# Kernel tuning notes

Hardware: AMD Instinct MI355X
Metric: run time of the kernel (lower is better)

The kernel has to match this reference:

```python
import jax, jax.numpy as jnp
import numpy as np

B, T = 128, 64          # batch, episode length
OB, AC, L, H = 32, 8, 128, 256  # ob_dim, ac_dim, latent_dim, mlp hidden
N_SUB = 4               # fixed Dopri5 substeps per interval (replaces adaptive PID controller)


def setup_inputs() -> dict:
    key = jax.random.key(0)
    ks = jax.random.split(key, 12)
    g = lambda k, shape, fan: jax.random.normal(k, shape, jnp.float32) / np.sqrt(fan)
    return {
        "ob": jax.random.normal(ks[0], (B, OB), jnp.float32),
        "acs": jax.random.normal(ks[1], (B, T, AC), jnp.float32),
        # strictly increasing timestamps (cumsum of uniform increments)
        "times": jnp.cumsum(jax.random.uniform(ks[2], (B, T), jnp.float32, 0.02, 0.1), axis=1),
        # ob encoder MLP (OB -> H -> L), relu hidden, identity out
        "We0": g(ks[3], (H, OB), OB), "be0": jnp.zeros((H,), jnp.float32),
        "We1": g(ks[4], (L, H), H), "be1": jnp.zeros((L,), jnp.float32),
        # latent dynamics MLP (L -> H -> H -> L)
        "Wd0": g(ks[5], (H, L), L), "bd0": jnp.zeros((H,), jnp.float32),
        "Wd1": g(ks[6], (H, H), H), "bd1": jnp.zeros((H,), jnp.float32),
        "Wd2": g(ks[7], (L, H), H), "bd2": jnp.zeros((L,), jnp.float32),
        # ob decoder MLP (L -> H -> OB)
        "Wo0": g(ks[8], (H, L), L), "bo0": jnp.zeros((H,), jnp.float32),
        "Wo1": g(ks[9], (OB, H), H), "bo1": jnp.zeros((OB,), jnp.float32),
        # GRU cell (input=AC, hidden=L), equinox layout: gates [r, z, n]
        "Wih": g(ks[10], (3 * L, AC), AC), "Whh": g(ks[11], (3 * L, L), L),
        "bih": jnp.zeros((3 * L,), jnp.float32), "bn": jnp.zeros((L,), jnp.float32),
    }


def reference(ob, acs, times, We0, be0, We1, be1, Wd0, bd0, Wd1, bd1, Wd2, bd2,
              Wo0, bo0, Wo1, bo1, Wih, Whh, bih, bn):
    def f(y):  # dynamics MLP on batched latent (B, L) -> (B, L)
        h1 = jax.nn.relu(y @ Wd0.T + bd0)
        h2 = jax.nn.relu(h1 @ Wd1.T + bd1)
        return h2 @ Wd2.T + bd2

    def gru(x, h):  # equinox GRUCell math, batched
        ir, iz, inn = jnp.split(x @ Wih.T + bih, 3, axis=-1)
        hr, hz, hn = jnp.split(h @ Whh.T, 3, axis=-1)
        r = jax.nn.sigmoid(ir + hr)
        z = jax.nn.sigmoid(iz + hz)
        n = jnp.tanh(inn + r * (hn + bn))
        return (1.0 - z) * n + z * h

    def dopri5_step(y, h):  # one Dopri5 (RK45) step, h: (B, 1) per-sample step size
        k1 = f(y)
        k2 = f(y + h * (0.2 * k1))
        k3 = f(y + h * (3/40 * k1 + 9/40 * k2))
        k4 = f(y + h * (44/45 * k1 - 56/15 * k2 + 32/9 * k3))
        k5 = f(y + h * (19372/6561 * k1 - 25360/2187 * k2 + 64448/6561 * k3 - 212/729 * k4))
        k6 = f(y + h * (9017/3168 * k1 - 355/33 * k2 + 46732/5247 * k3 + 49/176 * k4 - 5103/18656 * k5))
        return y + h * (35/384 * k1 + 500/1113 * k3 + 125/192 * k4 - 2187/6784 * k5 + 11/84 * k6)

    def integrate(y, dt):  # integrate latent ODE from 0 to dt with N_SUB fixed Dopri5 steps
        h = (dt / N_SUB)[:, None]
        return jax.lax.fori_loop(0, N_SUB, lambda i, yy: dopri5_step(yy, h), y)

    # encode first observation, consume first action
    latent0 = jax.nn.relu(ob @ We0.T + be0) @ We1.T + be1  # (B, L)
    latent0 = gru(acs[:, 0], latent0)

    dts = jnp.diff(times, axis=1)  # (B, T-1)

    def step(latent, xs):
        ac, dt = xs
        latent = integrate(latent, dt)
        latent = gru(ac, latent)
        return latent, latent

    xs = (jnp.swapaxes(acs[:, 1:], 0, 1), dts.T)  # time-major for scan
    _, lat_seq = jax.lax.scan(step, latent0, xs)  # (T-1, B, L)

    latents = jnp.concatenate([latent0[None], lat_seq], axis=0)  # (T, B, L)
    latents = jnp.swapaxes(latents, 0, 1)  # (B, T, L)

    h1 = jax.nn.relu(latents @ Wo0.T + bo0)
    return h1 @ Wo1.T + bo1  # (B, T, OB)
```

## Files before the change

kernel.cpp:

```cpp
#include <hip/hip_runtime.h>
#include <stdint.h>

#define NBATCH 128
#define NT     64
#define OBD    32
#define ACD    8
#define LDIM   128
#define HDIM   256

typedef _Float16 h2 __attribute__((ext_vector_type(2)));
typedef float    f4 __attribute__((ext_vector_type(4)));

#if defined(__has_builtin)
#  if __has_builtin(__builtin_amdgcn_fdot2)
#    define HAVE_FDOT2 1
#  endif
#endif

__device__ __forceinline__ float dot2f(h2 a, h2 b, float c) {
#ifdef HAVE_FDOT2
  return __builtin_amdgcn_fdot2(a, b, c, false);
#else
  return c + (float)a[0] * (float)b[0] + (float)a[1] * (float)b[1];
#endif
}

__device__ __forceinline__ h2 pkh(float a, float b) {
  h2 r; r[0] = (_Float16)a; r[1] = (_Float16)b; return r;
}

__device__ __forceinline__ h2 bch(float x) { return __builtin_bit_cast(h2, x); }

__device__ __forceinline__ float sigmf(float x) { return 1.0f / (1.0f + expf(-x)); }

#define DOT4(W, I, Q) \
    a0 = dot2f(W[4*(I)+0], bch(Q.x), a0); \
    a1 = dot2f(W[4*(I)+1], bch(Q.y), a1); \
    a2 = dot2f(W[4*(I)+2], bch(Q.z), a2); \
    a3 = dot2f(W[4*(I)+3], bch(Q.w), a3);

#define PI(i) ((i) + (((i) >> 5) << 2))
#define PA(i) ((i) + (((i) >> 6) << 2))
#define PB(i) ((i) + (((i) >> 5) << 2))

__global__ __attribute__((amdgpu_waves_per_eu(2, 2))) __launch_bounds__(512)
void ode_rnn_kernel(const float* __restrict__ ob,   const float* __restrict__ acs,
                    const float* __restrict__ times,
                    const float* __restrict__ We0,  const float* __restrict__ be0,
                    const float* __restrict__ We1,  const float* __restrict__ be1,
                    const float* __restrict__ Wd0,  const float* __restrict__ bd0,
                    const float* __restrict__ Wd1,  const float* __restrict__ bd1,
                    const float* __restrict__ Wd2,  const float* __restrict__ bd2,
                    const float* __restrict__ Wo0,  const float* __restrict__ bo0,
                    const float* __restrict__ Wo1,  const float* __restrict__ bo1,
                    const float* __restrict__ Wih,  const float* __restrict__ Whh,
                    const float* __restrict__ bih,  const float* __restrict__ bn,
                    float* __restrict__ out)
{
  const int t    = threadIdx.x;
  const int b    = blockIdx.x;
  const int p    = t >> 1;
  const int sub  = t & 1;
  const int r    = t >> 2;
  const int ksub = t & 3;

  __shared__ __align__(16) float s_lat[LDIM];
  __shared__ __align__(16) float s_gz[LDIM];
  __shared__ __align__(16) float s_gin[LDIM];
  __shared__ __align__(16) float s_ghn[LDIM];
  __shared__ __align__(16) float s_tmp[HDIM];
  __shared__ __align__(16) float s_obs[OBD];
  __shared__ __align__(16) float s_times[NT];
  __shared__ __align__(16) float s_acs[NT * ACD];
  __shared__ __align__(16) h2    s_in16[68];
  __shared__ __align__(16) h2    s_a16[132];
  __shared__ __align__(16) h2    s_b16[140];

  h2 w0[32], w1[64], w2[32];
  {
    const float2* pp = (const float2*)(Wd0 + p * LDIM + sub * 64);
#pragma unroll
    for (int i = 0; i < 32; ++i) { float2 v = pp[i]; w0[i] = pkh(v.x, v.y); }
  }
  {
    const float2* pp = (const float2*)(Wd1 + p * HDIM + sub * 128);
#pragma unroll
    for (int i = 0; i < 64; ++i) { float2 v = pp[i]; w1[i] = pkh(v.x, v.y); }
  }
  {
    const float2* pp = (const float2*)(Wd2 + r * HDIM + ksub * 64);
#pragma unroll
    for (int i = 0; i < 32; ++i) { float2 v = pp[i]; w2[i] = pkh(v.x, v.y); }
  }

  const float bb0 = bd0[p];
  const float bb1 = bd1[p];
  const float bb2 = bd2[r];
  const float rb0 = bo0[p];
  const float gA  = (t < 3 * LDIM) ? bih[t] : 0.0f;
  const float bnr = (t < LDIM) ? bn[t] : 0.0f;

  float latr = 0.0f;

  auto substep = [&](float hs) {
    float k0 = 0, k1 = 0, k2 = 0, k3 = 0, k4 = 0;
#pragma unroll
    for (int s = 0; s < 6; ++s) {
      float a0, a1, a2, a3, v;
      a0 = a1 = a2 = a3 = 0.0f;
      {
        const f4* src = ((const f4*)s_in16) + sub * 9;
#pragma unroll
        for (int i = 0; i < 8; ++i) { f4 q = src[i]; DOT4(w0, i, q) }
      }
      v = (a0 + a1) + (a2 + a3);
      v += __shfl_xor(v, 1);
      v = fmaxf(v + bb0, 0.0f);
      { float ov = __shfl_xor(v, 2); if ((t & 3) == 0) s_a16[PA(t >> 2)] = pkh(v, ov); }
      __syncthreads();
      a0 = a1 = a2 = a3 = 0.0f;
      {
        const f4* act = ((const f4*)s_a16) + sub * 17;
#pragma unroll
        for (int i = 0; i < 16; ++i) { f4 q = act[i]; DOT4(w1, i, q) }
      }
      v = (a0 + a1) + (a2 + a3);
      v += __shfl_xor(v, 1);
      v = fmaxf(v + bb1, 0.0f);
      { float ov = __shfl_xor(v, 2); if ((t & 3) == 0) s_b16[PB(t >> 2)] = pkh(v, ov); }
      __syncthreads();
      a0 = a1 = a2 = a3 = 0.0f;
      {
        const f4* src = ((const f4*)s_b16) + ksub * 9;
#pragma unroll
        for (int i = 0; i < 8; ++i) { f4 q = src[i]; DOT4(w2, i, q) }
      }
      v = (a0 + a1) + (a2 + a3);
      v += __shfl_xor(v, 1);
      v += __shfl_xor(v, 2);
      float kv = v + bb2;
      float z;
      if (s == 0) {
        k0 = kv; z = latr + hs * (0.2f * kv);
      } else if (s == 1) {
        k1 = kv; z = latr + hs * ((3.0f/40.0f)*k0 + (9.0f/40.0f)*kv);
      } else if (s == 2) {
        k2 = kv; z = latr + hs * ((44.0f/45.0f)*k0 - (56.0f/15.0f)*k1
                                + (32.0f/9.0f)*kv);
      } else if (s == 3) {
        k3 = kv; z = latr + hs * ((19372.0f/6561.0f)*k0 - (25360.0f/2187.0f)*k1
                                + (64448.0f/6561.0f)*k2 - (212.0f/729.0f)*kv);
      } else if (s == 4) {
        k4 = kv; z = latr + hs * ((9017.0f/3168.0f)*k0 - (355.0f/33.0f)*k1
                                + (46732.0f/5247.0f)*k2 + (49.0f/176.0f)*k3
                                - (5103.0f/18656.0f)*kv);
      } else {
        z = latr + hs * ((35.0f/384.0f)*k0 + (500.0f/1113.0f)*k2
                       + (125.0f/192.0f)*k3 - (2187.0f/6784.0f)*k4
                       + (11.0f/84.0f)*kv);
        latr = z;
      }
      { float ov = __shfl_xor(z, 4); if ((t & 7) == 0) s_in16[PI(t >> 3)] = pkh(z, ov); }
      if (s == 5 && ksub == 0) s_lat[r] = z;
      __syncthreads();
    }
  };

  auto gru = [&](int ts) {
    __syncthreads();
    float vi = gA, vh = 0.0f;
    if (t < 3 * LDIM) {
      const float* xa = s_acs + ts * ACD;
      const f4* wiv = (const f4*)(Wih + t * ACD);
      f4 wa = wiv[0], wb = wiv[1];
      vi += wa.x*xa[0] + wa.y*xa[1] + wa.z*xa[2] + wa.w*xa[3]
          + wb.x*xa[4] + wb.y*xa[5] + wb.z*xa[6] + wb.w*xa[7];
      const f4* wh = (const f4*)(Whh + t * LDIM);
      const f4* xl = (const f4*)s_lat;
#pragma unroll
      for (int k2 = 0; k2 < LDIM / 4; ++k2) {
        f4 w = wh[k2], x = xl[k2];
        vh += w.x*x.x + w.y*x.y + w.z*x.z + w.w*x.w;
      }
    }
    if (t >= LDIM && t < 2 * LDIM)          s_gz[t - LDIM] = vi + vh;
    else if (t >= 2 * LDIM && t < 3 * LDIM) { s_gin[t - 2*LDIM] = vi; s_ghn[t - 2*LDIM] = vh; }
    __syncthreads();
    if (t < LDIM) {
      float rg = sigmf(vi + vh);
      float zg = sigmf(s_gz[t]);
      float ng = tanhf(s_gin[t] + rg * (s_ghn[t] + bnr));
      float y  = (1.0f - zg) * ng + zg * s_lat[t];
      s_lat[t] = y;
      float ov = __shfl_xor(y, 1);
      if (!(t & 1)) s_in16[PI(t >> 1)] = pkh(y, ov);
    }
  };

  auto decode = [&](int ts) {
    __syncthreads();
    latr = s_lat[r];
    float acc = 0.0f;
    {
      const f4* wr = (const f4*)(Wo0 + p * LDIM + sub * 64);
      const f4* xl = ((const f4*)s_lat) + sub * 16;
#pragma unroll
      for (int k2 = 0; k2 < 16; ++k2) {
        f4 w = wr[k2], x = xl[k2];
        acc += w.x*x.x + w.y*x.y + w.z*x.z + w.w*x.w;
      }
    }
    acc += __shfl_xor(acc, 1);
    acc = fmaxf(acc + rb0, 0.0f);
    { float ov = __shfl_xor(acc, 2); if ((t & 3) == 0) s_a16[PA(t >> 2)] = pkh(acc, ov); }
    __syncthreads();
    const int o  = t >> 4;
    const int sl = t & 15;
    float v2 = 0.0f;
    {
      const f4* wr = (const f4*)(Wo1 + o * HDIM + sl * 16);
      const h2* xs = s_a16 + sl * 8 + ((sl >> 3) << 2);
#pragma unroll
      for (int i = 0; i < 4; ++i) {
        f4 w = wr[i];
        h2 xa = xs[2*i], xb = xs[2*i+1];
        v2 += w.x*(float)xa[0] + w.y*(float)xa[1]
            + w.z*(float)xb[0] + w.w*(float)xb[1];
      }
    }
    v2 += __shfl_xor(v2, 1);
    v2 += __shfl_xor(v2, 2);
    v2 += __shfl_xor(v2, 4);
    v2 += __shfl_xor(v2, 8);
    if (sl == 0) out[((size_t)b * NT + ts) * OBD + o] = v2 + bo1[o];
    __syncthreads();
  };

  if (t < OBD) s_obs[t] = ob[b * OBD + t];
  if (t < NT)  s_times[t] = times[b * NT + t];
  s_acs[t] = acs[(size_t)b * NT * ACD + t];
  __syncthreads();
  if (t < HDIM) {
    float acc = be0[t];
    const float* wr = We0 + t * OBD;
#pragma unroll
    for (int j = 0; j < OBD; ++j) acc += wr[j] * s_obs[j];
    s_tmp[t] = fmaxf(acc, 0.0f);
  }
  __syncthreads();
  {
    const f4* wr = (const f4*)(We1 + r * HDIM + ksub * 64);
    const f4* xs = ((const f4*)s_tmp) + ksub * 16;
    float acc = 0.0f;
#pragma unroll
    for (int k = 0; k < 16; ++k) {
      f4 w = wr[k], x = xs[k];
      acc += w.x*x.x + w.y*x.y + w.z*x.z + w.w*x.w;
    }
    acc += __shfl_xor(acc, 1);
    acc += __shfl_xor(acc, 2);
    if (ksub == 0) s_lat[r] = acc + be1[r];
  }

  gru(0);
  decode(0);

#pragma unroll 1
  for (int ts = 1; ts < NT; ++ts) {
    float hs = 0.25f * (s_times[ts] - s_times[ts - 1]);
#pragma unroll 1
    for (int su = 0; su < 4; ++su) substep(hs);
    gru(ts);
    decode(ts);
  }
}

extern "C" void kernel_launch(void* const* d_in, const int* in_sizes, int n_in,
                              void* d_out, int out_size, void* d_ws, size_t ws_size,
                              hipStream_t stream) {
  (void)in_sizes; (void)n_in; (void)d_ws; (void)ws_size; (void)out_size;
  const float* ob    = (const float*)d_in[0];
  const float* acs   = (const float*)d_in[1];
  const float* times = (const float*)d_in[2];
  const float* We0   = (const float*)d_in[3];
  const float* be0   = (const float*)d_in[4];
  const float* We1   = (const float*)d_in[5];
  const float* be1   = (const float*)d_in[6];
  const float* Wd0   = (const float*)d_in[7];
  const float* bd0   = (const float*)d_in[8];
  const float* Wd1   = (const float*)d_in[9];
  const float* bd1   = (const float*)d_in[10];
  const float* Wd2   = (const float*)d_in[11];
  const float* bd2   = (const float*)d_in[12];
  const float* Wo0   = (const float*)d_in[13];
  const float* bo0   = (const float*)d_in[14];
  const float* Wo1   = (const float*)d_in[15];
  const float* bo1   = (const float*)d_in[16];
  const float* Wih   = (const float*)d_in[17];
  const float* Whh   = (const float*)d_in[18];
  const float* bih   = (const float*)d_in[19];
  const float* bn    = (const float*)d_in[20];

  ode_rnn_kernel<<<dim3(NBATCH), dim3(512), 0, stream>>>(
      ob, acs, times, We0, be0, We1, be1, Wd0, bd0, Wd1, bd1, Wd2, bd2,
      Wo0, bo0, Wo1, bo1, Wih, Whh, bih, bn, (float*)d_out);
}
```

Baseline: 2.345 ms.

## Stream fp16 Wd1 weights from a pre-packed workspace instead of registers

Adds a prep kernel that converts Wd1 to packed fp16 in a coalesced, thread-interleaved layout in the workspace. The main kernel no longer keeps the 64-register Wd1 slice resident and instead reloads it from global memory (L2/L1) on every dynamics evaluation, with loads software-pipelined ahead of the dot products. This frees VGPRs to reduce spilling or register pressure. The cost is repeated global-memory traffic inside the serial ODE loop, plus the latency of those loads.

```diff
diff --git a/kernel.cpp b/kernel.cpp
--- a/kernel.cpp
+++ b/kernel.cpp
@@ -30,6 +30,7 @@
 }
 
 __device__ __forceinline__ h2 bch(float x) { return __builtin_bit_cast(h2, x); }
+__device__ __forceinline__ float fch(h2 x) { return __builtin_bit_cast(float, x); }
 
 __device__ __forceinline__ float sigmf(float x) { return 1.0f / (1.0f + expf(-x)); }
 
@@ -42,6 +43,19 @@
 #define PI(i) ((i) + (((i) >> 5) << 2))
 #define PA(i) ((i) + (((i) >> 6) << 2))
 #define PB(i) ((i) + (((i) >> 5) << 2))
+
+__global__ void prep_w1(const float* __restrict__ Wd1, f4* __restrict__ ws4) {
+  int idx = blockIdx.x * blockDim.x + threadIdx.x;
+  int j  = idx >> 9;
+  int tt = idx & 511;
+  const float* src = Wd1 + (tt >> 1) * HDIM + (tt & 1) * 128 + j * 8;
+  f4 c;
+  c.x = fch(pkh(src[0], src[1]));
+  c.y = fch(pkh(src[2], src[3]));
+  c.z = fch(pkh(src[4], src[5]));
+  c.w = fch(pkh(src[6], src[7]));
+  ws4[j * 512 + tt] = c;
+}
 
 __global__ __attribute__((amdgpu_waves_per_eu(2, 2))) __launch_bounds__(512)
 void ode_rnn_kernel(const float* __restrict__ ob,   const float* __restrict__ acs,
@@ -49,12 +63,13 @@
                     const float* __restrict__ We0,  const float* __restrict__ be0,
                     const float* __restrict__ We1,  const float* __restrict__ be1,
                     const float* __restrict__ Wd0,  const float* __restrict__ bd0,
-                    const float* __restrict__ Wd1,  const float* __restrict__ bd1,
+                    const float* __restrict__ bd1,
                     const float* __restrict__ Wd2,  const float* __restrict__ bd2,
                     const float* __restrict__ Wo0,  const float* __restrict__ bo0,
                     const float* __restrict__ Wo1,  const float* __restrict__ bo1,
                     const float* __restrict__ Wih,  const float* __restrict__ Whh,
                     const float* __restrict__ bih,  const float* __restrict__ bn,
+                    const f4* __restrict__ ws4,
                     float* __restrict__ out)
 {
   const int t    = threadIdx.x;
@@ -76,22 +91,18 @@
   __shared__ __align__(16) h2    s_a16[132];
   __shared__ __align__(16) h2    s_b16[140];
 
-  h2 w0[32], w1[64], w2[32];
+  h2 w0[32], w2[32];
   {
     const float2* pp = (const float2*)(Wd0 + p * LDIM + sub * 64);
 #pragma unroll
     for (int i = 0; i < 32; ++i) { float2 v = pp[i]; w0[i] = pkh(v.x, v.y); }
   }
   {
-    const float2* pp = (const float2*)(Wd1 + p * HDIM + sub * 128);
-#pragma unroll
-    for (int i = 0; i < 64; ++i) { float2 v = pp[i]; w1[i] = pkh(v.x, v.y); }
-  }
-  {
     const float2* pp = (const float2*)(Wd2 + r * HDIM + ksub * 64);
 #pragma unroll
     for (int i = 0; i < 32; ++i) { float2 v = pp[i]; w2[i] = pkh(v.x, v.y); }
   }
+  const f4* wsb = ws4 + t;
 
   const float bb0 = bd0[p];
   const float bb1 = bd1[p];
@@ -107,6 +118,8 @@
 #pragma unroll
     for (int s = 0; s < 6; ++s) {
       float a0, a1, a2, a3, v;
+      f4 y0 = wsb[0 * 512], y1 = wsb[1 * 512];
+      f4 y2 = wsb[2 * 512], y3 = wsb[3 * 512];
       a0 = a1 = a2 = a3 = 0.0f;
       {
         const f4* src = ((const f4*)s_in16) + sub * 9;
@@ -121,8 +134,27 @@
       a0 = a1 = a2 = a3 = 0.0f;
       {
         const f4* act = ((const f4*)s_a16) + sub * 17;
-#pragma unroll
-        for (int i = 0; i < 16; ++i) { f4 q = act[i]; DOT4(w1, i, q) }
+        f4 q;
+#define SDOT(WV, J) q = act[J]; \
+        a0 = dot2f(bch(WV.x), bch(q.x), a0); \
+        a1 = dot2f(bch(WV.y), bch(q.y), a1); \
+        a2 = dot2f(bch(WV.z), bch(q.z), a2); \
+        a3 = dot2f(bch(WV.w), bch(q.w), a3);
+        f4 y4 = wsb[4 * 512],  y5 = wsb[5 * 512];
+        SDOT(y0, 0)  SDOT(y1, 1)
+        f4 y6 = wsb[6 * 512],  y7 = wsb[7 * 512];
+        SDOT(y2, 2)  SDOT(y3, 3)
+        f4 y8 = wsb[8 * 512],  y9 = wsb[9 * 512];
+        SDOT(y4, 4)  SDOT(y5, 5)
+        f4 y10 = wsb[10 * 512], y11 = wsb[11 * 512];
+        SDOT(y6, 6)  SDOT(y7, 7)
+        f4 y12 = wsb[12 * 512], y13 = wsb[13 * 512];
+        SDOT(y8, 8)  SDOT(y9, 9)
+        f4 y14 = wsb[14 * 512], y15 = wsb[15 * 512];
+        SDOT(y10, 10) SDOT(y11, 11)
+        SDOT(y12, 12) SDOT(y13, 13)
+        SDOT(y14, 14) SDOT(y15, 15)
+#undef SDOT
       }
       v = (a0 + a1) + (a2 + a3);
       v += __shfl_xor(v, 1);
@@ -278,7 +310,7 @@
 extern "C" void kernel_launch(void* const* d_in, const int* in_sizes, int n_in,
                               void* d_out, int out_size, void* d_ws, size_t ws_size,
                               hipStream_t stream) {
-  (void)in_sizes; (void)n_in; (void)d_ws; (void)ws_size; (void)out_size;
+  (void)in_sizes; (void)n_in; (void)ws_size; (void)out_size;
   const float* ob    = (const float*)d_in[0];
   const float* acs   = (const float*)d_in[1];
   const float* times = (const float*)d_in[2];
@@ -301,7 +333,10 @@
   const float* bih   = (const float*)d_in[19];
   const float* bn    = (const float*)d_in[20];
 
+  f4* ws4 = (f4*)d_ws;
+
+  prep_w1<<<dim3(16), dim3(512), 0, stream>>>(Wd1, ws4);
   ode_rnn_kernel<<<dim3(NBATCH), dim3(512), 0, stream>>>(
-      ob, acs, times, We0, be0, We1, be1, Wd0, bd0, Wd1, bd1, Wd2, bd2,
-      Wo0, bo0, Wo1, bo1, Wih, Whh, bih, bn, (float*)d_out);
-}
+      ob, acs, times, We0, be0, We1, be1, Wd0, bd0, bd1, Wd2, bd2,
+      Wo0, bo0, Wo1, bo1, Wih, Whh, bih, bn, ws4, (float*)d_out);
+}
```

Result: no change. 2.314 ms (median of 2 runs) (-1.3%).
